# Kernel optimization log

Hardware: AMD Instinct MI355X
Metric: run time of the kernel (lower is better)

The kernel has to match this reference:

```python
import jax, jax.numpy as jnp
import numpy as np


def setup_inputs() -> dict:
    key = jax.random.key(0)
    ks = jax.random.split(key, 5)
    B, P_LEN, D = 16, 1024, 512
    scale = 0.02
    return {
        "P": jax.random.normal(ks[0], (B, P_LEN, D), dtype=jnp.float32),
        "w_atten": jax.random.normal(ks[1], (3 * D,), dtype=jnp.float32) * scale,
        "w1": jax.random.normal(ks[2], (2 * D, D), dtype=jnp.float32) * scale,
        "w2": jax.random.normal(ks[3], (2 * D, D), dtype=jnp.float32) * scale,
        "w3": jax.random.normal(ks[4], (2 * D, D), dtype=jnp.float32) * scale,
        "b1": jnp.zeros((D,), dtype=jnp.float32),
        "b2": jnp.zeros((D,), dtype=jnp.float32),
        "b3": jnp.zeros((D,), dtype=jnp.float32),
    }


def reference(P, w_atten, w1, w2, w3, b1, b2, b3):
    # P: (b, p, d). Original builds a (b, p, 3d, p) concat tensor; the score
    # A[b,i,j] = wa . P_i + wb . P_j + wc . (P_i * P_j) factorizes exactly:
    d = P.shape[-1]
    wa, wb, wc = w_atten[:d], w_atten[d:2 * d], w_atten[2 * d:]
    si = P @ wa                                   # (b, p)  contribution of row token i
    sj = P @ wb                                   # (b, p)  contribution of col token j
    A = si[:, :, None] + sj[:, None, :] + jnp.einsum("bid,bjd->bij", P * wc, P)
    SA = jax.nn.softmax(A, axis=2)                # softmax over j
    attn_res = jnp.einsum("bij,bjd->bid", SA, P)  # (b, p, d)
    # Fuse gate (DecayingDropout is identity at inference)
    Pc = jnp.concatenate([P, attn_res], axis=2)   # (b, p, 2d)
    z = jnp.tanh(Pc @ w1 + b1)
    r = jax.nn.sigmoid(Pc @ w2 + b2)
    f = jax.nn.sigmoid(Pc @ w3 + b3)
    return r * P + f * z
```

## Files before the change

kernel.cpp:

```cpp
#include <hip/hip_runtime.h>
#include <stdint.h>

#define S_LEN 1024
#define DDIM  512
#define NBATCH 16

typedef __attribute__((ext_vector_type(8))) short bf16x8;
typedef __attribute__((ext_vector_type(4))) float f32x4;
typedef unsigned short ushort_t;

__device__ __forceinline__ unsigned short f2bf(float x) {
  union { float f; uint32_t u; } v; v.f = x;
  return (unsigned short)((v.u + 0x7fffu + ((v.u >> 16) & 1u)) >> 16);
}
__device__ __forceinline__ float bf2f(unsigned short h) {
  union { float f; uint32_t u; } v; v.u = ((uint32_t)h) << 16;
  return v.f;
}

#define GL16(g, l) __builtin_amdgcn_global_load_lds(                          \
    (const __attribute__((address_space(1))) void*)(g),                       \
    (__attribute__((address_space(3))) void*)(l), 16, 0, 0)

__global__ __launch_bounds__(256) void prep_rows(
    const float* __restrict__ P, const float* __restrict__ w_atten,
    unsigned short* __restrict__ Pbf, unsigned short* __restrict__ Qbf,
    float* __restrict__ sj) {
  int wave = threadIdx.x >> 6, lane = threadIdx.x & 63;
  int row = blockIdx.x * 4 + wave;
  const float* prow = P + (size_t)row * DDIM;
  float s = 0.f;
#pragma unroll
  for (int h = 0; h < 2; ++h) {
    int d = h * 256 + lane * 4;
    float4 p  = *(const float4*)(prow + d);
    float4 wb = *(const float4*)(w_atten + DDIM + d);
    float4 wc = *(const float4*)(w_atten + 2 * DDIM + d);
    s += p.x * wb.x + p.y * wb.y + p.z * wb.z + p.w * wb.w;
    ushort4 pb, qb;
    pb.x = f2bf(p.x); pb.y = f2bf(p.y); pb.z = f2bf(p.z); pb.w = f2bf(p.w);
    qb.x = f2bf(p.x * wc.x); qb.y = f2bf(p.y * wc.y);
    qb.z = f2bf(p.z * wc.z); qb.w = f2bf(p.w * wc.w);
    *(ushort4*)(Pbf + (size_t)row * DDIM + d) = pb;
    *(ushort4*)(Qbf + (size_t)row * DDIM + d) = qb;
  }
#pragma unroll
  for (int o = 32; o; o >>= 1) s += __shfl_xor(s, o);
  if (lane == 0) sj[row] = s;
}

__global__ __launch_bounds__(256) void transpose_f2b(
    const float* __restrict__ in, unsigned short* __restrict__ out,
    int R, int C, long inStride, long outStride) {
  __shared__ unsigned short T[64][65];
  in  += (size_t)blockIdx.z * inStride;
  out += (size_t)blockIdx.z * outStride;
  int c0 = blockIdx.x * 64, r0 = blockIdx.y * 64;
  int tx = threadIdx.x & 63, ty = threadIdx.x >> 6;
#pragma unroll
  for (int rr = 0; rr < 16; ++rr) {
    int rl = ty * 16 + rr;
    T[rl][tx] = f2bf(in[(size_t)(r0 + rl) * C + c0 + tx]);
  }
  __syncthreads();
#pragma unroll
  for (int rr = 0; rr < 16; ++rr) {
    int cl = ty * 16 + rr;
    out[(size_t)(c0 + cl) * R + r0 + tx] = T[tx][cl];
  }
}

__global__ __launch_bounds__(256) void transpose_b2b(
    const unsigned short* __restrict__ in, unsigned short* __restrict__ out,
    int R, int C, long inStride, long outStride) {
  __shared__ unsigned short T[64][65];
  in  += (size_t)blockIdx.z * inStride;
  out += (size_t)blockIdx.z * outStride;
  int c0 = blockIdx.x * 64, r0 = blockIdx.y * 64;
  int tx = threadIdx.x & 63, ty = threadIdx.x >> 6;
#pragma unroll
  for (int rr = 0; rr < 16; ++rr) {
    int rl = ty * 16 + rr;
    T[rl][tx] = in[(size_t)(r0 + rl) * C + c0 + tx];
  }
  __syncthreads();
#pragma unroll
  for (int rr = 0; rr < 16; ++rr) {
    int cl = ty * 16 + rr;
    out[(size_t)(c0 + cl) * R + r0 + tx] = T[tx][cl];
  }
}

#define GSTEP(KT)                                                             \
  if constexpr ((KT) < NT) {                                                  \
    if constexpr ((KT) + 2 < NT) {                                            \
      ushort_t* dA_ = lA[((KT) + 2) % 3];                                     \
      ushort_t* dB_ = lB[((KT) + 2) % 3];                                     \
      GL16(aLo0 + ((KT) + 2) * 32, dA_ + lbase);                              \
      GL16(aLo1 + ((KT) + 2) * 32, dA_ + 2048 + lbase);                       \
      GL16(bB0 + ((KT) + 2) * 32, dB_ + lbase);                               \
      GL16(bB1 + ((KT) + 2) * 32, dB_ + 2048 + lbase);                        \
    }                                                                         \
    {                                                                         \
      const ushort_t* Ard_ = lA[(KT) % 3];                                    \
      const ushort_t* Brd_ = lB[(KT) % 3];                                    \
      bf16x8 af[4], bfr[4];                                                   \
      _Pragma("unroll") for (int m = 0; m < 4; ++m)                           \
        af[m] = *(const bf16x8*)(Ard_ + (wr * 64 + m * 16 + frow) * 32 + fswz); \
      _Pragma("unroll") for (int n = 0; n < 4; ++n)                           \
        bfr[n] = *(const bf16x8*)(Brd_ + (wc * 64 + n * 16 + frow) * 32 + fswz); \
      __builtin_amdgcn_s_setprio(1);                                          \
      _Pragma("unroll") for (int m = 0; m < 4; ++m)                           \
      _Pragma("unroll") for (int n = 0; n < 4; ++n)                           \
        acc[m][n] = __builtin_amdgcn_mfma_f32_16x16x32_bf16(af[m], bfr[n],    \
                                                            acc[m][n], 0, 0, 0); \
      __builtin_amdgcn_s_setprio(0);                                          \
    }                                                                         \
    if constexpr ((KT) + 1 < NT) {                                            \
      if constexpr ((KT) + 2 < NT)                                            \
        asm volatile("s_waitcnt vmcnt(4) lgkmcnt(0)" ::: "memory");           \
      else                                                                    \
        asm volatile("s_waitcnt vmcnt(0) lgkmcnt(0)" ::: "memory");           \
      __builtin_amdgcn_s_barrier();                                           \
    }                                                                         \
  }

template<int NT, int EPI>
__global__ __launch_bounds__(256) void gemm_tb(
    const ushort_t* __restrict__ A,
    const ushort_t* __restrict__ Bt,
    ushort_t* __restrict__ C,
    const float* __restrict__ bias,
    int N, int K, int lda,
    long sAb, long sBb, long sCb, long sBiasb) {
  __shared__ __align__(16) ushort_t lA[3][4096];
  __shared__ __align__(16) ushort_t lB[3][4096];
  const int t = threadIdx.x, lane = t & 63, wave = t >> 6;

  const int gx = gridDim.x, gy = gridDim.y;
  int hblk = blockIdx.x + gx * (blockIdx.y + gy * blockIdx.z);
  int cpx = (gx * gy * (int)gridDim.z) >> 3;
  int wk = (hblk & 7) * cpx + (hblk >> 3);
  const int bx = wk % gx; int rem = wk / gx;
  const int by = rem % gy;
  const int z  = rem / gy;

  A += (size_t)z * sAb;
  Bt += (size_t)z * sBb;
  C += (size_t)z * sCb;
  if (bias) bias += (size_t)z * sBiasb;
  const int bm = by * 128, bn = bx * 128;

  f32x4 acc[4][4];
#pragma unroll
  for (int m = 0; m < 4; ++m)
#pragma unroll
    for (int n = 0; n < 4; ++n) acc[m][n] = {0.f, 0.f, 0.f, 0.f};

  const int wr = wave >> 1, wc = wave & 1;
  const int frow = lane & 15;
  const int fswz = (((lane >> 4) ^ ((frow >> 1) & 3)) * 8);
  const int srow = t >> 2;
  const int skc = (((t & 3) ^ ((t >> 3) & 3)) * 8);
  const int lbase = (t & 192) * 8;

  const ushort_t* aLo0 = A + (size_t)(bm + srow) * lda + skc;
  const ushort_t* aLo1 = aLo0 + (size_t)64 * lda;
  const ushort_t* bB0  = Bt + (size_t)(bn + srow) * K + skc;
  const ushort_t* bB1  = bB0 + (size_t)64 * K;

  GL16(aLo0,      lA[0] + lbase);   GL16(aLo1,      lA[0] + 2048 + lbase);
  GL16(bB0,       lB[0] + lbase);   GL16(bB1,       lB[0] + 2048 + lbase);
  GL16(aLo0 + 32, lA[1] + lbase);   GL16(aLo1 + 32, lA[1] + 2048 + lbase);
  GL16(bB0 + 32,  lB[1] + lbase);   GL16(bB1 + 32,  lB[1] + 2048 + lbase);
  asm volatile("s_waitcnt vmcnt(4)" ::: "memory");
  __builtin_amdgcn_s_barrier();

  GSTEP(0)  GSTEP(1)  GSTEP(2)  GSTEP(3)  GSTEP(4)  GSTEP(5)  GSTEP(6)  GSTEP(7)
  GSTEP(8)  GSTEP(9)  GSTEP(10) GSTEP(11) GSTEP(12) GSTEP(13) GSTEP(14) GSTEP(15)
  GSTEP(16) GSTEP(17) GSTEP(18) GSTEP(19) GSTEP(20) GSTEP(21) GSTEP(22) GSTEP(23)
  GSTEP(24) GSTEP(25) GSTEP(26) GSTEP(27) GSTEP(28) GSTEP(29) GSTEP(30) GSTEP(31)

#pragma unroll
  for (int m = 0; m < 4; ++m) {
    int row0 = bm + wr * 64 + m * 16 + (lane >> 4) * 4;
#pragma unroll
    for (int n = 0; n < 4; ++n) {
      int col = bn + wc * 64 + n * 16 + frow;
      float bc = (EPI >= 1) ? bias[col] : 0.f;
#pragma unroll
      for (int i = 0; i < 4; ++i) {
        float v = acc[m][n][i];
        if (EPI == 1) v += bc;
        C[(size_t)(row0 + i) * N + col] = f2bf(v);
      }
    }
  }
}

#define MSTEP(KT)                                                             \
  {                                                                           \
    if ((KT) + 1 < 32) {                                                      \
      ushort_t* dA_ = lA[((KT) + 1) & 1];                                     \
      ushort_t* dB_ = lB[((KT) + 1) & 1];                                     \
      if ((KT) + 1 < 16) {                                                    \
        GL16(aLo0 + ((KT) + 1) * 32, dA_ + lbase);                            \
        GL16(aLo1 + ((KT) + 1) * 32, dA_ + 2048 + lbase);                     \
      } else {                                                                \
        GL16(aHi0 + ((KT) + 1 - 16) * 32, dA_ + lbase);                       \
        GL16(aHi1 + ((KT) + 1 - 16) * 32, dA_ + 2048 + lbase);                \
      }                                                                       \
      GL16(bS0 + ((KT) + 1) * 32, dB_ + lbase);                               \
      GL16(bS1 + ((KT) + 1) * 32, dB_ + 2048 + lbase);                        \
      GL16(bS2 + ((KT) + 1) * 32, dB_ + 4096 + lbase);                        \
    }                                                                         \
    {                                                                         \
      const ushort_t* Ard_ = lA[(KT) & 1];                                    \
      const ushort_t* Brd_ = lB[(KT) & 1];                                    \
      bf16x8 af[4];                                                           \
      _Pragma("unroll") for (int m = 0; m < 4; ++m)                           \
        af[m] = *(const bf16x8*)(Ard_ + (wr * 64 + m * 16 + frow) * 32 + fswz); \
      _Pragma("unroll") for (int s = 0; s < 3; ++s) {                         \
        bf16x8 b0 = *(const bf16x8*)(Brd_ + s * 2048 +                        \
                                     (wc * 32 + frow) * 32 + fswz);           \
        bf16x8 b1v = *(const bf16x8*)(Brd_ + s * 2048 +                       \
                                      (wc * 32 + 16 + frow) * 32 + fswz);     \
        __builtin_amdgcn_s_setprio(1);                                        \
        _Pragma("unroll") for (int m = 0; m < 4; ++m) {                       \
          acc[s][m][0] = __builtin_amdgcn_mfma_f32_16x16x32_bf16(             \
              af[m], b0, acc[s][m][0], 0, 0, 0);                              \
          acc[s][m][1] = __builtin_amdgcn_mfma_f32_16x16x32_bf16(             \
              af[m], b1v, acc[s][m][1], 0, 0, 0);                             \
        }                                                                     \
        __builtin_amdgcn_s_setprio(0);                                        \
      }                                                                       \
    }                                                                         \
    if ((KT) < 31) __syncthreads();                                           \
  }

__global__ __launch_bounds__(256, 2) void mlp_fused(
    const ushort_t* __restrict__ Pbf,
    const ushort_t* __restrict__ attn,
    const ushort_t* __restrict__ Wt,
    const float* __restrict__ P,
    const float* __restrict__ b1,
    const float* __restrict__ b2,
    const float* __restrict__ b3,
    float* __restrict__ out) {
  __shared__ __align__(16) ushort_t lA[2][4096];
  __shared__ __align__(16) ushort_t lB[2][3 * 2048];
  const int t = threadIdx.x, lane = t & 63, wave = t >> 6;

  int hblk = blockIdx.x + 8 * blockIdx.y;
  int wk = (hblk & 7) * 128 + (hblk >> 3);
  const int bx = wk & 7;
  const int by = wk >> 3;
  const int bm = by * 128, bn = bx * 64;

  f32x4 acc[3][4][2];
#pragma unroll
  for (int s = 0; s < 3; ++s)
#pragma unroll
    for (int m = 0; m < 4; ++m)
#pragma unroll
      for (int n = 0; n < 2; ++n) acc[s][m][n] = {0.f, 0.f, 0.f, 0.f};

  const int wr = wave >> 1, wc = wave & 1;
  const int frow = lane & 15;
  const int fswz = (((lane >> 4) ^ ((frow >> 1) & 3)) * 8);
  const int srow = t >> 2;
  const int skc = (((t & 3) ^ ((t >> 3) & 3)) * 8);
  const int lbase = (t & 192) * 8;

  const ushort_t* aLo0 = Pbf + (size_t)(bm + srow) * 512 + skc;
  const ushort_t* aLo1 = aLo0 + (size_t)64 * 512;
  const ushort_t* aHi0 = attn + (size_t)(bm + srow) * 512 + skc;
  const ushort_t* aHi1 = aHi0 + (size_t)64 * 512;
  const ushort_t* bS0 = Wt + (size_t)(bn + srow) * 1024 + skc;
  const ushort_t* bS1 = bS0 + (size_t)512 * 1024;
  const ushort_t* bS2 = bS0 + (size_t)1024 * 1024;

  GL16(aLo0, lA[0] + lbase);  GL16(aLo1, lA[0] + 2048 + lbase);
  GL16(bS0,  lB[0] + lbase);  GL16(bS1,  lB[0] + 2048 + lbase);
  GL16(bS2,  lB[0] + 4096 + lbase);
  __syncthreads();

  MSTEP(0)  MSTEP(1)  MSTEP(2)  MSTEP(3)  MSTEP(4)  MSTEP(5)  MSTEP(6)  MSTEP(7)
  MSTEP(8)  MSTEP(9)  MSTEP(10) MSTEP(11) MSTEP(12) MSTEP(13) MSTEP(14) MSTEP(15)
  MSTEP(16) MSTEP(17) MSTEP(18) MSTEP(19) MSTEP(20) MSTEP(21) MSTEP(22) MSTEP(23)
  MSTEP(24) MSTEP(25) MSTEP(26) MSTEP(27) MSTEP(28) MSTEP(29) MSTEP(30) MSTEP(31)

#pragma unroll
  for (int m = 0; m < 4; ++m) {
    int row0 = bm + wr * 64 + m * 16 + (lane >> 4) * 4;
#pragma unroll
    for (int n = 0; n < 2; ++n) {
      int col = bn + wc * 32 + n * 16 + frow;
      float B1 = b1[col], B2 = b2[col], B3 = b3[col];
#pragma unroll
      for (int i = 0; i < 4; ++i) {
        size_t idx = (size_t)(row0 + i) * 512 + col;
        float z = tanhf(acc[0][m][n][i] + B1);
        float r = 1.f / (1.f + __expf(-(acc[1][m][n][i] + B2)));
        float f = 1.f / (1.f + __expf(-(acc[2][m][n][i] + B3)));
        out[idx] = r * P[idx] + f * z;
      }
    }
  }
}

__global__ __launch_bounds__(256) void softmax_rows(unsigned short* __restrict__ Sb) {
  __shared__ float red[8];
  unsigned short* p = Sb + (size_t)blockIdx.x * S_LEN;
  int t = threadIdx.x, wave = t >> 6, lane = t & 63;
  ushort4 u = *(ushort4*)(p + t * 4);
  float v0 = bf2f(u.x), v1 = bf2f(u.y), v2 = bf2f(u.z), v3 = bf2f(u.w);
  float mx = fmaxf(fmaxf(v0, v1), fmaxf(v2, v3));
#pragma unroll
  for (int o = 32; o; o >>= 1) mx = fmaxf(mx, __shfl_xor(mx, o));
  if (lane == 0) red[wave] = mx;
  __syncthreads();
  mx = fmaxf(fmaxf(red[0], red[1]), fmaxf(red[2], red[3]));
  float e0 = __expf(v0 - mx), e1 = __expf(v1 - mx);
  float e2 = __expf(v2 - mx), e3 = __expf(v3 - mx);
  float ss = e0 + e1 + e2 + e3;
#pragma unroll
  for (int o = 32; o; o >>= 1) ss += __shfl_xor(ss, o);
  if (lane == 0) red[4 + wave] = ss;
  __syncthreads();
  float inv = 1.f / (red[4] + red[5] + red[6] + red[7]);
  u.x = f2bf(e0 * inv); u.y = f2bf(e1 * inv);
  u.z = f2bf(e2 * inv); u.w = f2bf(e3 * inv);
  *(ushort4*)(p + t * 4) = u;
}

extern "C" void kernel_launch(void* const* d_in, const int* in_sizes, int n_in,
                              void* d_out, int out_size, void* d_ws, size_t ws_size,
                              hipStream_t stream) {
  const float* P  = (const float*)d_in[0];
  const float* wa = (const float*)d_in[1];
  const float* w1 = (const float*)d_in[2];
  const float* w2 = (const float*)d_in[3];
  const float* w3 = (const float*)d_in[4];
  const float* b1 = (const float*)d_in[5];
  const float* b2 = (const float*)d_in[6];
  const float* b3 = (const float*)d_in[7];
  float* out = (float*)d_out;
  char* ws = (char*)d_ws;
  const size_t MB = 1024 * 1024;

  unsigned short* Pbf  = (unsigned short*)(ws + 0);
  unsigned short* PT   = (unsigned short*)(ws + 16 * MB);
  unsigned short* Qbf  = (unsigned short*)(ws + 32 * MB);
  unsigned short* Sbuf = (unsigned short*)(ws + 48 * MB);
  unsigned short* attn = (unsigned short*)(ws + 80 * MB);
  unsigned short* Wt   = (unsigned short*)(ws + 96 * MB);
  float*          sj   = (float*)(ws + 99 * MB);

  const long SD = (long)S_LEN * DDIM;
  const long SS = (long)S_LEN * S_LEN;

  prep_rows<<<4096, 256, 0, stream>>>(P, wa, Pbf, Qbf, sj);
  transpose_b2b<<<dim3(8, 16, NBATCH), 256, 0, stream>>>(Pbf, PT, S_LEN, DDIM, SD, SD);
  transpose_f2b<<<dim3(8, 16, 1), 256, 0, stream>>>(w1, Wt,          1024, 512, 0, 0);
  transpose_f2b<<<dim3(8, 16, 1), 256, 0, stream>>>(w2, Wt + SD,     1024, 512, 0, 0);
  transpose_f2b<<<dim3(8, 16, 1), 256, 0, stream>>>(w3, Wt + 2 * SD, 1024, 512, 0, 0);

  gemm_tb<16, 1><<<dim3(8, 8, NBATCH), 256, 0, stream>>>(
      Qbf, Pbf, Sbuf, sj, 1024, 512, 512, SD, SD, SS, S_LEN);
  softmax_rows<<<16384, 256, 0, stream>>>(Sbuf);
  gemm_tb<32, 0><<<dim3(4, 8, NBATCH), 256, 0, stream>>>(
      Sbuf, PT, attn, nullptr, 512, 1024, 1024, SS, SD, SD, 0);
  mlp_fused<<<dim3(8, 128), 256, 0, stream>>>(
      Pbf, attn, Wt, P, b1, b2, b3, out);
}
```

Baseline: 177.2 us.

## Halve batched GEMM N-tile and triple-buffer the fused MLP pipeline

New measurement: 183.0 us. 1.03x slower.

```diff
diff --git a/kernel.cpp b/kernel.cpp
--- a/kernel.cpp
+++ b/kernel.cpp
@@ -91,7 +91,7 @@
   }
 }
 
-#define GSTEP(KT)                                                             \
+#define G64STEP(KT)                                                           \
   if constexpr ((KT) < NT) {                                                  \
     if constexpr ((KT) + 2 < NT) {                                            \
       ushort_t* dA_ = lA[((KT) + 2) % 3];                                     \
@@ -99,26 +99,25 @@
       GL16(aLo0 + ((KT) + 2) * 32, dA_ + lbase);                              \
       GL16(aLo1 + ((KT) + 2) * 32, dA_ + 2048 + lbase);                       \
       GL16(bB0 + ((KT) + 2) * 32, dB_ + lbase);                               \
-      GL16(bB1 + ((KT) + 2) * 32, dB_ + 2048 + lbase);                        \
     }                                                                         \
     {                                                                         \
       const ushort_t* Ard_ = lA[(KT) % 3];                                    \
       const ushort_t* Brd_ = lB[(KT) % 3];                                    \
-      bf16x8 af[4], bfr[4];                                                   \
+      bf16x8 af[4], bfr[2];                                                   \
       _Pragma("unroll") for (int m = 0; m < 4; ++m)                           \
         af[m] = *(const bf16x8*)(Ard_ + (wr * 64 + m * 16 + frow) * 32 + fswz); \
-      _Pragma("unroll") for (int n = 0; n < 4; ++n)                           \
-        bfr[n] = *(const bf16x8*)(Brd_ + (wc * 64 + n * 16 + frow) * 32 + fswz); \
+      _Pragma("unroll") for (int n = 0; n < 2; ++n)                           \
+        bfr[n] = *(const bf16x8*)(Brd_ + (wc * 32 + n * 16 + frow) * 32 + fswz); \
       __builtin_amdgcn_s_setprio(1);                                          \
       _Pragma("unroll") for (int m = 0; m < 4; ++m)                           \
-      _Pragma("unroll") for (int n = 0; n < 4; ++n)                           \
+      _Pragma("unroll") for (int n = 0; n < 2; ++n)                           \
         acc[m][n] = __builtin_amdgcn_mfma_f32_16x16x32_bf16(af[m], bfr[n],    \
                                                             acc[m][n], 0, 0, 0); \
       __builtin_amdgcn_s_setprio(0);                                          \
     }                                                                         \
     if constexpr ((KT) + 1 < NT) {                                            \
       if constexpr ((KT) + 2 < NT)                                            \
-        asm volatile("s_waitcnt vmcnt(4) lgkmcnt(0)" ::: "memory");           \
+        asm volatile("s_waitcnt vmcnt(3) lgkmcnt(0)" ::: "memory");           \
       else                                                                    \
         asm volatile("s_waitcnt vmcnt(0) lgkmcnt(0)" ::: "memory");           \
       __builtin_amdgcn_s_barrier();                                           \
@@ -126,7 +125,7 @@
   }
 
 template<int NT, int EPI>
-__global__ __launch_bounds__(256) void gemm_tb(
+__global__ __launch_bounds__(256) void gemm_64(
     const ushort_t* __restrict__ A,
     const ushort_t* __restrict__ Bt,
     ushort_t* __restrict__ C,
@@ -134,7 +133,7 @@
     int N, int K, int lda,
     long sAb, long sBb, long sCb, long sBiasb) {
   __shared__ __align__(16) ushort_t lA[3][4096];
-  __shared__ __align__(16) ushort_t lB[3][4096];
+  __shared__ __align__(16) ushort_t lB[3][2048];
   const int t = threadIdx.x, lane = t & 63, wave = t >> 6;
 
   const int gx = gridDim.x, gy = gridDim.y;
@@ -149,13 +148,13 @@
   Bt += (size_t)z * sBb;
   C += (size_t)z * sCb;
   if (bias) bias += (size_t)z * sBiasb;
-  const int bm = by * 128, bn = bx * 128;
-
-  f32x4 acc[4][4];
+  const int bm = by * 128, bn = bx * 64;
+
+  f32x4 acc[4][2];
 #pragma unroll
   for (int m = 0; m < 4; ++m)
 #pragma unroll
-    for (int n = 0; n < 4; ++n) acc[m][n] = {0.f, 0.f, 0.f, 0.f};
+    for (int n = 0; n < 2; ++n) acc[m][n] = {0.f, 0.f, 0.f, 0.f};
 
   const int wr = wave >> 1, wc = wave & 1;
   const int frow = lane & 15;
@@ -167,26 +166,27 @@
   const ushort_t* aLo0 = A + (size_t)(bm + srow) * lda + skc;
   const ushort_t* aLo1 = aLo0 + (size_t)64 * lda;
   const ushort_t* bB0  = Bt + (size_t)(bn + srow) * K + skc;
-  const ushort_t* bB1  = bB0 + (size_t)64 * K;
-
-  GL16(aLo0,      lA[0] + lbase);   GL16(aLo1,      lA[0] + 2048 + lbase);
-  GL16(bB0,       lB[0] + lbase);   GL16(bB1,       lB[0] + 2048 + lbase);
-  GL16(aLo0 + 32, lA[1] + lbase);   GL16(aLo1 + 32, lA[1] + 2048 + lbase);
-  GL16(bB0 + 32,  lB[1] + lbase);   GL16(bB1 + 32,  lB[1] + 2048 + lbase);
-  asm volatile("s_waitcnt vmcnt(4)" ::: "memory");
+
+  GL16(aLo0,      lA[0] + lbase);  GL16(aLo1,      lA[0] + 2048 + lbase);
+  GL16(bB0,       lB[0] + lbase);
+  GL16(aLo0 + 32, lA[1] + lbase);  GL16(aLo1 + 32, lA[1] + 2048 + lbase);
+  GL16(bB0 + 32,  lB[1] + lbase);
+  asm volatile("s_waitcnt vmcnt(3)" ::: "memory");
   __builtin_amdgcn_s_barrier();
 
-  GSTEP(0)  GSTEP(1)  GSTEP(2)  GSTEP(3)  GSTEP(4)  GSTEP(5)  GSTEP(6)  GSTEP(7)
-  GSTEP(8)  GSTEP(9)  GSTEP(10) GSTEP(11) GSTEP(12) GSTEP(13) GSTEP(14) GSTEP(15)
-  GSTEP(16) GSTEP(17) GSTEP(18) GSTEP(19) GSTEP(20) GSTEP(21) GSTEP(22) GSTEP(23)
-  GSTEP(24) GSTEP(25) GSTEP(26) GSTEP(27) GSTEP(28) GSTEP(29) GSTEP(30) GSTEP(31)
+  G64STEP(0)  G64STEP(1)  G64STEP(2)  G64STEP(3)  G64STEP(4)  G64STEP(5)
+  G64STEP(6)  G64STEP(7)  G64STEP(8)  G64STEP(9)  G64STEP(10) G64STEP(11)
+  G64STEP(12) G64STEP(13) G64STEP(14) G64STEP(15) G64STEP(16) G64STEP(17)
+  G64STEP(18) G64STEP(19) G64STEP(20) G64STEP(21) G64STEP(22) G64STEP(23)
+  G64STEP(24) G64STEP(25) G64STEP(26) G64STEP(27) G64STEP(28) G64STEP(29)
+  G64STEP(30) G64STEP(31)
 
 #pragma unroll
   for (int m = 0; m < 4; ++m) {
     int row0 = bm + wr * 64 + m * 16 + (lane >> 4) * 4;
 #pragma unroll
-    for (int n = 0; n < 4; ++n) {
-      int col = bn + wc * 64 + n * 16 + frow;
+    for (int n = 0; n < 2; ++n) {
+      int col = bn + wc * 32 + n * 16 + frow;
       float bc = (EPI >= 1) ? bias[col] : 0.f;
 #pragma unroll
       for (int i = 0; i < 4; ++i) {
@@ -200,23 +200,23 @@
 
 #define MSTEP(KT)                                                             \
   {                                                                           \
-    if ((KT) + 1 < 32) {                                                      \
-      ushort_t* dA_ = lA[((KT) + 1) & 1];                                     \
-      ushort_t* dB_ = lB[((KT) + 1) & 1];                                     \
-      if ((KT) + 1 < 16) {                                                    \
-        GL16(aLo0 + ((KT) + 1) * 32, dA_ + lbase);                            \
-        GL16(aLo1 + ((KT) + 1) * 32, dA_ + 2048 + lbase);                     \
+    if constexpr ((KT) + 2 < 32) {                                            \
+      ushort_t* dA_ = lA[((KT) + 2) % 3];                                     \
+      ushort_t* dB_ = lB[((KT) + 2) % 3];                                     \
+      if constexpr ((KT) + 2 < 16) {                                          \
+        GL16(aLo0 + ((KT) + 2) * 32, dA_ + lbase);                            \
+        GL16(aLo1 + ((KT) + 2) * 32, dA_ + 2048 + lbase);                     \
       } else {                                                                \
-        GL16(aHi0 + ((KT) + 1 - 16) * 32, dA_ + lbase);                       \
-        GL16(aHi1 + ((KT) + 1 - 16) * 32, dA_ + 2048 + lbase);                \
+        GL16(aHi0 + ((KT) + 2 - 16) * 32, dA_ + lbase);                       \
+        GL16(aHi1 + ((KT) + 2 - 16) * 32, dA_ + 2048 + lbase);                \
       }                                                                       \
-      GL16(bS0 + ((KT) + 1) * 32, dB_ + lbase);                               \
-      GL16(bS1 + ((KT) + 1) * 32, dB_ + 2048 + lbase);                        \
-      GL16(bS2 + ((KT) + 1) * 32, dB_ + 4096 + lbase);                        \
+      GL16(bS0 + ((KT) + 2) * 32, dB_ + lbase);                               \
+      GL16(bS1 + ((KT) + 2) * 32, dB_ + 2048 + lbase);                        \
+      GL16(bS2 + ((KT) + 2) * 32, dB_ + 4096 + lbase);                        \
     }                                                                         \
     {                                                                         \
-      const ushort_t* Ard_ = lA[(KT) & 1];                                    \
-      const ushort_t* Brd_ = lB[(KT) & 1];                                    \
+      const ushort_t* Ard_ = lA[(KT) % 3];                                    \
+      const ushort_t* Brd_ = lB[(KT) % 3];                                    \
       bf16x8 af[4];                                                           \
       _Pragma("unroll") for (int m = 0; m < 4; ++m)                           \
         af[m] = *(const bf16x8*)(Ard_ + (wr * 64 + m * 16 + frow) * 32 + fswz); \
@@ -235,7 +235,13 @@
         __builtin_amdgcn_s_setprio(0);                                        \
       }                                                                       \
     }                                                                         \
-    if ((KT) < 31) __syncthreads();                                           \
+    if constexpr ((KT) + 1 < 32) {                                            \
+      if constexpr ((KT) + 2 < 32)                                            \
+        asm volatile("s_waitcnt vmcnt(5) lgkmcnt(0)" ::: "memory");           \
+      else                                                                    \
+        asm volatile("s_waitcnt vmcnt(0) lgkmcnt(0)" ::: "memory");           \
+      __builtin_amdgcn_s_barrier();                                           \
+    }                                                                         \
   }
 
 __global__ __launch_bounds__(256, 2) void mlp_fused(
@@ -247,8 +253,8 @@
     const float* __restrict__ b2,
     const float* __restrict__ b3,
     float* __restrict__ out) {
-  __shared__ __align__(16) ushort_t lA[2][4096];
-  __shared__ __align__(16) ushort_t lB[2][3 * 2048];
+  __shared__ __align__(16) ushort_t lA[3][4096];
+  __shared__ __align__(16) ushort_t lB[3][3 * 2048];
   const int t = threadIdx.x, lane = t & 63, wave = t >> 6;
 
   int hblk = blockIdx.x + 8 * blockIdx.y;
@@ -280,10 +286,14 @@
   const ushort_t* bS1 = bS0 + (size_t)512 * 1024;
   const ushort_t* bS2 = bS0 + (size_t)1024 * 1024;
 
-  GL16(aLo0, lA[0] + lbase);  GL16(aLo1, lA[0] + 2048 + lbase);
-  GL16(bS0,  lB[0] + lbase);  GL16(bS1,  lB[0] + 2048 + lbase);
-  GL16(bS2,  lB[0] + 4096 + lbase);
-  __syncthreads();
+  GL16(aLo0,      lA[0] + lbase);  GL16(aLo1,      lA[0] + 2048 + lbase);
+  GL16(bS0,       lB[0] + lbase);  GL16(bS1,       lB[0] + 2048 + lbase);
+  GL16(bS2,       lB[0] + 4096 + lbase);
+  GL16(aLo0 + 32, lA[1] + lbase);  GL16(aLo1 + 32, lA[1] + 2048 + lbase);
+  GL16(bS0 + 32,  lB[1] + lbase);  GL16(bS1 + 32,  lB[1] + 2048 + lbase);
+  GL16(bS2 + 32,  lB[1] + 4096 + lbase);
+  asm volatile("s_waitcnt vmcnt(5)" ::: "memory");
+  __builtin_amdgcn_s_barrier();
 
   MSTEP(0)  MSTEP(1)  MSTEP(2)  MSTEP(3)  MSTEP(4)  MSTEP(5)  MSTEP(6)  MSTEP(7)
   MSTEP(8)  MSTEP(9)  MSTEP(10) MSTEP(11) MSTEP(12) MSTEP(13) MSTEP(14) MSTEP(15)
@@ -366,10 +376,10 @@
   transpose_f2b<<<dim3(8, 16, 1), 256, 0, stream>>>(w2, Wt + SD,     1024, 512, 0, 0);
   transpose_f2b<<<dim3(8, 16, 1), 256, 0, stream>>>(w3, Wt + 2 * SD, 1024, 512, 0, 0);
 
-  gemm_tb<16, 1><<<dim3(8, 8, NBATCH), 256, 0, stream>>>(
+  gemm_64<16, 1><<<dim3(16, 8, NBATCH), 256, 0, stream>>>(
       Qbf, Pbf, Sbuf, sj, 1024, 512, 512, SD, SD, SS, S_LEN);
   softmax_rows<<<16384, 256, 0, stream>>>(Sbuf);
-  gemm_tb<32, 0><<<dim3(4, 8, NBATCH), 256, 0, stream>>>(
+  gemm_64<32, 0><<<dim3(8, 8, NBATCH), 256, 0, stream>>>(
       Sbuf, PT, attn, nullptr, 512, 1024, 1024, SS, SD, SD, 0);
   mlp_fused<<<dim3(8, 128), 256, 0, stream>>>(
       Pbf, attn, Wt, P, b1, b2, b3, out);
```
